# Optimization experiments

Measured on AMD Instinct MI355X. Metric: run time of the kernel, lower is better.

## Reference

```python
import jax, jax.numpy as jnp
import numpy as np

B, T, D, H, E, K, F = 8, 1024, 512, 8, 8, 2, 2048
HD = D // H
EPS = 1e-5


def _layernorm(x, g, b):
    m = jnp.mean(x, axis=-1, keepdims=True)
    v = jnp.mean((x - m) ** 2, axis=-1, keepdims=True)
    return (x - m) * jax.lax.rsqrt(v + EPS) * g + b


def setup_inputs() -> dict:
    key = jax.random.key(0)
    ks = jax.random.split(key, 12)
    s = lambda d: 1.0 / np.sqrt(d)
    return {
        "x": jax.random.normal(ks[0], (B, T, D), jnp.float32),
        "ln1_g": jnp.ones((D,), jnp.float32),
        "ln1_b": jnp.zeros((D,), jnp.float32),
        "ln2_g": jnp.ones((D,), jnp.float32),
        "ln2_b": jnp.zeros((D,), jnp.float32),
        "Wqkv": jax.random.normal(ks[1], (D, 3 * D), jnp.float32) * s(D),
        "bqkv": jnp.zeros((3 * D,), jnp.float32),
        "Wo": jax.random.normal(ks[2], (D, D), jnp.float32) * s(D),
        "bo": jnp.zeros((D,), jnp.float32),
        "Wg": jax.random.normal(ks[3], (D, E), jnp.float32) * s(D),
        "We1": jax.random.normal(ks[4], (E, D, F), jnp.float32) * s(D),
        "be1": jnp.zeros((E, F), jnp.float32),
        "We2": jax.random.normal(ks[5], (E, F, D), jnp.float32) * s(F),
        "be2": jnp.zeros((E, D), jnp.float32),
    }


def _attn(x, Wqkv, bqkv, Wo, bo):
    qkv = x @ Wqkv + bqkv                      # [B,T,3D]
    q, k, v = jnp.split(qkv, 3, axis=-1)
    q = q.reshape(B, T, H, HD)
    k = k.reshape(B, T, H, HD)
    v = v.reshape(B, T, H, HD)
    scores = jnp.einsum("bqhd,bkhd->bhqk", q, k) / np.sqrt(HD)
    causal = jnp.tril(jnp.ones((T, T), bool))
    scores = jnp.where(causal, scores, jnp.finfo(scores.dtype).min)
    p = jax.nn.softmax(scores, axis=-1)
    o = jnp.einsum("bhqk,bkhd->bqhd", p, v).reshape(B, T, D)
    return o @ Wo + bo


def _moe(h, Wg, We1, be1, We2, be2):
    hf = h.reshape(-1, D)                      # [N,D]
    N = hf.shape[0]
    probs = jax.nn.softmax(hf @ Wg, axis=-1)   # [N,E]
    topw, topi = jax.lax.top_k(probs, K)       # [N,K]
    topw = topw / jnp.sum(topw, axis=-1, keepdims=True)
    gates = jnp.zeros((N, E), hf.dtype).at[jnp.arange(N)[:, None], topi].add(topw)
    out = jnp.zeros_like(hf)
    for e in range(E):                         # fixed small expert loop
        hid = jax.nn.gelu(hf @ We1[e] + be1[e])
        out = out + gates[:, e:e + 1] * (hid @ We2[e] + be2[e])
    return out.reshape(h.shape)


def reference(x, ln1_g, ln1_b, ln2_g, ln2_b, Wqkv, bqkv, Wo, bo, Wg, We1, be1, We2, be2):
    # Pipeline chunking over batch is a scheduling detail; math is the plain block.
    h = x + _attn(_layernorm(x, ln1_g, ln1_b), Wqkv, bqkv, Wo, bo)
    return h + _moe(_layernorm(h, ln2_g, ln2_b), Wg, We1, be1, We2, be2)
```

## Files before the change

### kernel.cpp

```cpp
#include <hip/hip_runtime.h>


typedef unsigned short u16;
typedef unsigned int   u32;
typedef unsigned long long u64;
typedef __attribute__((ext_vector_type(8))) short short8;
typedef __attribute__((ext_vector_type(4))) float f32x4;

#define DEV static __device__ __forceinline__

DEV u16 f2bf(float f){
  union { float f; u32 u; } x; x.f = f;
  return (u16)((x.u + 0x7FFFu + ((x.u >> 16) & 1u)) >> 16);
}
DEV float bf2f(u16 b){
  union { u32 u; float f; } x; x.u = ((u32)b) << 16; return x.f;
}
DEV f32x4 mfma16(short8 a, short8 b, f32x4 c){
  return __builtin_amdgcn_mfma_f32_16x16x32_bf16(a, b, c, 0, 0, 0);
}
DEV void g2l16(const void* g, void* l){
  __builtin_amdgcn_global_load_lds((const __attribute__((address_space(1))) u32*)g,
                                   (__attribute__((address_space(3))) u32*)l, 16, 0, 0);
}
DEV void wait_vm0(){ asm volatile("s_waitcnt vmcnt(0)" ::: "memory"); }

__global__ __launch_bounds__(256) void transpose_cvt2(const float* __restrict__ src,
    u16* __restrict__ dh, u16* __restrict__ dl, int R, int C)
{
  __shared__ float tile[32][33];
  const size_t zb = (size_t)blockIdx.z * R * C;
  src += zb; dh += zb; dl += zb;
  const int tx = threadIdx.x, ty = threadIdx.y;
  const int c0 = blockIdx.x * 32, r0 = blockIdx.y * 32;
  #pragma unroll
  for (int i = 0; i < 4; ++i)
    tile[ty + i*8][tx] = src[(size_t)(r0 + ty + i*8) * C + c0 + tx];
  __syncthreads();
  #pragma unroll
  for (int i = 0; i < 4; ++i){
    float v = tile[tx][ty + i*8];
    size_t o = (size_t)(c0 + ty + i*8) * R + r0 + tx;
    u16 hb = f2bf(v);
    dh[o] = hb;
    dl[o] = f2bf(v - bf2f(hb));
  }
}

__global__ __launch_bounds__(256) void transpose_cvt1(const float* __restrict__ src,
    u16* __restrict__ d, int R, int C)
{
  __shared__ float tile[32][33];
  const size_t zb = (size_t)blockIdx.z * R * C;
  src += zb; d += zb;
  const int tx = threadIdx.x, ty = threadIdx.y;
  const int c0 = blockIdx.x * 32, r0 = blockIdx.y * 32;
  #pragma unroll
  for (int i = 0; i < 4; ++i)
    tile[ty + i*8][tx] = src[(size_t)(r0 + ty + i*8) * C + c0 + tx];
  __syncthreads();
  #pragma unroll
  for (int i = 0; i < 4; ++i)
    d[(size_t)(c0 + ty + i*8) * R + r0 + tx] = f2bf(tile[tx][ty + i*8]);
}

__global__ __launch_bounds__(256) void ln1_kernel(const float* __restrict__ x,
    const float* __restrict__ g, const float* __restrict__ b,
    u16* __restrict__ yh, u16* __restrict__ yl)
{
  const int wid = threadIdx.x >> 6, lane = threadIdx.x & 63;
  const int row = blockIdx.x * 4 + wid;
  const float* xr = x + (size_t)row * 512 + lane * 8;
  f32x4 t0 = ((const f32x4*)xr)[0], t1 = ((const f32x4*)xr)[1];
  float v[8];
  #pragma unroll
  for (int j = 0; j < 8; ++j) v[j] = (j < 4) ? t0[j] : t1[j-4];
  float s = 0.f, q = 0.f;
  #pragma unroll
  for (int j = 0; j < 8; ++j){ s += v[j]; q += v[j]*v[j]; }
  #pragma unroll
  for (int o = 32; o; o >>= 1){ s += __shfl_xor(s, o); q += __shfl_xor(q, o); }
  const float mean = s * (1.f/512.f);
  const float var  = q * (1.f/512.f) - mean*mean;
  const float rstd = rsqrtf(var + 1e-5f);
  f32x4 g0 = ((const f32x4*)(g + lane*8))[0], g1 = ((const f32x4*)(g + lane*8))[1];
  f32x4 b0 = ((const f32x4*)(b + lane*8))[0], b1 = ((const f32x4*)(b + lane*8))[1];
  short8 vh, vl;
  #pragma unroll
  for (int j = 0; j < 8; ++j){
    float gg = (j < 4) ? g0[j] : g1[j-4];
    float bb = (j < 4) ? b0[j] : b1[j-4];
    float y = (v[j]-mean)*rstd*gg + bb;
    u16 hb = f2bf(y);
    vh[j] = (short)hb;
    vl[j] = (short)f2bf(y - bf2f(hb));
  }
  ((short8*)(yh + (size_t)row*512 + lane*8))[0] = vh;
  ((short8*)(yl + (size_t)row*512 + lane*8))[0] = vl;
}

template<int MODE>
__global__ __launch_bounds__(256) void gemm_split2(
    const u16* __restrict__ Ah, const u16* __restrict__ Al,
    const u16* __restrict__ Bh, const u16* __restrict__ Bl,
    const float* __restrict__ bias, int K,
    u16* __restrict__ q_h, u16* __restrict__ q_l, u16* __restrict__ q_m,
    u16* __restrict__ k_h, u16* __restrict__ k_l, u16* __restrict__ k_m,
    u16* __restrict__ v_h, u16* __restrict__ v_l,
    const float* __restrict__ xres, float* __restrict__ hout)
{
  __shared__ u16 Ash[2][128*32], Asl[2][128*32], Bsh[2][128*32], Bsl[2][128*32];
  const int tid = threadIdx.x;
  const int wid = tid >> 6, lane = tid & 63;
  const int wr = wid >> 1, wc = wid & 1;
  const int lr = lane & 15, lg = lane >> 4;
  const int m0 = blockIdx.x * 128, n0 = blockIdx.y * 128;

  size_t aoff[2], boff[2];
  u32 ldso[2];
  #pragma unroll
  for (int r = 0; r < 2; ++r){
    int i = r*256 + tid;
    int row = i >> 2, cc = i & 3;
    int scc = cc ^ (row & 3);
    aoff[r] = ((size_t)(m0+row)*K + scc*8) * 2;
    boff[r] = ((size_t)(n0+row)*K + scc*8) * 2;
    ldso[r] = (u32)(r*256 + wid*64) * 8;
  }

  f32x4 acc[4][4];
  #pragma unroll
  for (int a = 0; a < 4; ++a)
    #pragma unroll
    for (int b = 0; b < 4; ++b) acc[a][b] = 0;

  const char* pAh = (const char*)Ah; const char* pAl = (const char*)Al;
  const char* pBh = (const char*)Bh; const char* pBl = (const char*)Bl;

  auto stage = [&](int sb, int ks){
    const size_t kb = (size_t)ks * 64;
    #pragma unroll
    for (int r = 0; r < 2; ++r){
      g2l16(pAh + aoff[r] + kb, &Ash[sb][0] + ldso[r]);
      g2l16(pAl + aoff[r] + kb, &Asl[sb][0] + ldso[r]);
      g2l16(pBh + boff[r] + kb, &Bsh[sb][0] + ldso[r]);
      g2l16(pBl + boff[r] + kb, &Bsl[sb][0] + ldso[r]);
    }
  };

  const int nks = K >> 5;
  stage(0, 0);
  wait_vm0();
  __syncthreads();
  int buf = 0;
  for (int ks = 0; ks < nks; ++ks){
    if (ks + 1 < nks) stage(buf ^ 1, ks + 1);
    short8 ah[4], al[4], bh[4], bl[4];
    #pragma unroll
    for (int mt = 0; mt < 4; ++mt){
      int row = wr*64 + mt*16 + lr;
      int kcs = lg ^ (row & 3);
      int o = row*32 + kcs*8;
      ah[mt] = *(const short8*)(&Ash[buf][0] + o);
      al[mt] = *(const short8*)(&Asl[buf][0] + o);
    }
    #pragma unroll
    for (int nt = 0; nt < 4; ++nt){
      int row = wc*64 + nt*16 + lr;
      int kcs = lg ^ (row & 3);
      int o = row*32 + kcs*8;
      bh[nt] = *(const short8*)(&Bsh[buf][0] + o);
      bl[nt] = *(const short8*)(&Bsl[buf][0] + o);
    }
    __builtin_amdgcn_s_setprio(1);
    #pragma unroll
    for (int mt = 0; mt < 4; ++mt)
      #pragma unroll
      for (int nt = 0; nt < 4; ++nt){
        f32x4 c = acc[mt][nt];
        c = mfma16(ah[mt], bh[nt], c);
        c = mfma16(ah[mt], bl[nt], c);
        c = mfma16(al[mt], bh[nt], c);
        acc[mt][nt] = c;
      }
    __builtin_amdgcn_s_setprio(0);
    wait_vm0();
    __syncthreads();
    buf ^= 1;
  }

  #pragma unroll
  for (int mt = 0; mt < 4; ++mt){
    #pragma unroll
    for (int nt = 0; nt < 4; ++nt){
      const int col = n0 + wc*64 + nt*16 + lr;
      const float bv = bias[col];
      #pragma unroll
      for (int r2 = 0; r2 < 4; ++r2){
        const int row = m0 + wr*64 + mt*16 + 4*lg + r2;
        const float val = acc[mt][nt][r2] + bv;
        if constexpr (MODE == 0){
          const int which = col >> 9, rem = col & 511;
          const int hh = rem >> 6, hd = rem & 63;
          const int b_ = row >> 10, t_ = row & 1023;
          const size_t idx = ((size_t)(b_*8 + hh)*1024 + t_)*64 + hd;
          const u16 hb = f2bf(val);
          if (which == 2){
            v_h[idx] = hb;
            v_l[idx] = f2bf(val - bf2f(hb));
          } else {
            const float r1 = val - bf2f(hb);
            const u16 lb = f2bf(r1);
            const u16 mb = f2bf(r1 - bf2f(lb));
            if (which == 0){ q_h[idx]=hb; q_l[idx]=lb; q_m[idx]=mb; }
            else           { k_h[idx]=hb; k_l[idx]=lb; k_m[idx]=mb; }
          }
        } else {
          const size_t o = (size_t)row*512 + col;
          hout[o] = val + xres[o];
        }
      }
    }
  }
}

__global__ __launch_bounds__(256) void attn_kernel(
    const u16* __restrict__ q_h, const u16* __restrict__ q_l, const u16* __restrict__ q_m,
    const u16* __restrict__ k_h, const u16* __restrict__ k_l, const u16* __restrict__ k_m,
    const u16* __restrict__ v_h, const u16* __restrict__ v_l,
    u16* __restrict__ aoh, u16* __restrict__ aol)
{
  __shared__ u16 Ksh[64*64], Ksl[64*64], Ksm[64*64];
  __shared__ u16 Vth[64*72], Vtl[64*72];
  __shared__ u16 Ph[4*16*72], Pl[4*16*72];
  const int tid = threadIdx.x, wid = tid >> 6, lane = tid & 63;
  const int lr = lane & 15, lg = lane >> 4;
  const int bfl = blockIdx.x;
  const int xcd = bfl & 7, jj_ = bfl >> 3;
  const int bh = xcd * 8 + (jj_ & 7);
  const int qt = 15 - (jj_ >> 3);
  const int q0 = qt * 64;
  const size_t base = (size_t)bh * 1024 * 64;

  short8 qfh[2], qfl[2], qfm[2];
  {
    const int qrow = q0 + wid*16 + lr;
    #pragma unroll
    for (int c = 0; c < 2; ++c){
      const size_t o = base + (size_t)qrow*64 + c*32 + lg*8;
      qfh[c] = *(const short8*)(q_h + o);
      qfl[c] = *(const short8*)(q_l + o);
      qfm[c] = *(const short8*)(q_m + o);
    }
  }
  f32x4 oacc[4];
  float m_r[4], l_r[4];
  #pragma unroll
  for (int nt = 0; nt < 4; ++nt) oacc[nt] = 0;
  #pragma unroll
  for (int r = 0; r < 4; ++r){ m_r[r] = -1e30f; l_r[r] = 0.f; }

  short8 kreg[3][2];
  short8 vreg[2][2];
  const int pp = tid & 31, d0 = (tid >> 5) * 8;

  auto load_tile = [&](int kt){
    #pragma unroll
    for (int r = 0; r < 2; ++r){
      const int i = r*256 + tid;
      const int row = i >> 3, cc = i & 7;
      const int scc = cc ^ (row & 7);
      const size_t go = base + (size_t)(kt*64 + row)*64 + scc*8;
      kreg[0][r] = *(const short8*)(k_h + go);
      kreg[1][r] = *(const short8*)(k_l + go);
      kreg[2][r] = *(const short8*)(k_m + go);
    }
    const size_t g0 = base + (size_t)(kt*64 + 2*pp)*64 + d0;
    vreg[0][0] = *(const short8*)(v_h + g0);
    vreg[0][1] = *(const short8*)(v_h + g0 + 64);
    vreg[1][0] = *(const short8*)(v_l + g0);
    vreg[1][1] = *(const short8*)(v_l + g0 + 64);
  };

  load_tile(0);
  for (int kt = 0; kt <= qt; ++kt){
    if (kt) __syncthreads();
    #pragma unroll
    for (int r = 0; r < 2; ++r){
      const int o = (r*256 + tid) * 8;
      *(short8*)(Ksh + o) = kreg[0][r];
      *(short8*)(Ksl + o) = kreg[1][r];
      *(short8*)(Ksm + o) = kreg[2][r];
    }
    #pragma unroll
    for (int j = 0; j < 8; ++j){
      u32 ph_ = (u32)(u16)vreg[0][0][j] | ((u32)(u16)vreg[0][1][j] << 16);
      u32 pl_ = (u32)(u16)vreg[1][0][j] | ((u32)(u16)vreg[1][1][j] << 16);
      *(u32*)(Vth + (d0+j)*72 + 2*pp) = ph_;
      *(u32*)(Vtl + (d0+j)*72 + 2*pp) = pl_;
    }
    __syncthreads();
    if (kt < qt) load_tile(kt + 1);
    __builtin_amdgcn_sched_barrier(0);

    f32x4 s[4];
    #pragma unroll
    for (int nt = 0; nt < 4; ++nt) s[nt] = 0;
    __builtin_amdgcn_s_setprio(1);
    #pragma unroll
    for (int c = 0; c < 2; ++c){
      #pragma unroll
      for (int nt = 0; nt < 4; ++nt){
        const int row = nt*16 + lr;
        const int kcs = (c*4 + lg) ^ (row & 7);
        const int o = row*64 + kcs*8;
        short8 kh_ = *(const short8*)(Ksh + o);
        short8 kl_ = *(const short8*)(Ksl + o);
        short8 km_ = *(const short8*)(Ksm + o);
        f32x4 cacc = s[nt];
        cacc = mfma16(qfh[c], kh_, cacc);
        cacc = mfma16(qfh[c], kl_, cacc);
        cacc = mfma16(qfl[c], kh_, cacc);
        cacc = mfma16(qfh[c], km_, cacc);
        cacc = mfma16(qfm[c], kh_, cacc);
        cacc = mfma16(qfl[c], kl_, cacc);
        s[nt] = cacc;
      }
    }
    __builtin_amdgcn_s_setprio(0);
    float sc[4][4];
    const bool last = (kt == qt);
    #pragma unroll
    for (int nt = 0; nt < 4; ++nt)
      #pragma unroll
      for (int r = 0; r < 4; ++r){
        float v = s[nt][r] * 0.125f;
        if (last){
          int qa = q0 + wid*16 + 4*lg + r;
          int ka = kt*64 + nt*16 + lr;
          if (ka > qa) v = -1e30f;
        }
        sc[nt][r] = v;
      }
    float pr[4][4];
    #pragma unroll
    for (int r = 0; r < 4; ++r){
      float mx = fmaxf(fmaxf(sc[0][r], sc[1][r]), fmaxf(sc[2][r], sc[3][r]));
      #pragma unroll
      for (int o2 = 8; o2; o2 >>= 1) mx = fmaxf(mx, __shfl_xor(mx, o2));
      const float nm = fmaxf(m_r[r], mx);
      const float al = __expf(m_r[r] - nm);
      float sum = 0.f;
      #pragma unroll
      for (int nt = 0; nt < 4; ++nt){
        float e_ = __expf(sc[nt][r] - nm);
        pr[nt][r] = e_;
        sum += e_;
      }
      #pragma unroll
      for (int o2 = 8; o2; o2 >>= 1) sum += __shfl_xor(sum, o2);
      l_r[r] = l_r[r]*al + sum;
      m_r[r] = nm;
      #pragma unroll
      for (int nt = 0; nt < 4; ++nt) oacc[nt][r] *= al;
    }
    #pragma unroll
    for (int nt = 0; nt < 4; ++nt)
      #pragma unroll
      for (int r = 0; r < 4; ++r){
        const float pv = pr[nt][r];
        const u16 hb = f2bf(pv);
        const u16 lb = f2bf(pv - bf2f(hb));
        const int o = wid*1152 + (4*lg + r)*72 + nt*16 + lr;
        Ph[o] = hb; Pl[o] = lb;
      }
    #pragma unroll
    for (int c = 0; c < 2; ++c){
      const int po = wid*1152 + lr*72 + c*32 + lg*8;
      short8 pah = *(const short8*)(Ph + po);
      short8 pal = *(const short8*)(Pl + po);
      __builtin_amdgcn_s_setprio(1);
      #pragma unroll
      for (int nt = 0; nt < 4; ++nt){
        const int vo = (nt*16 + lr)*72 + c*32 + lg*8;
        short8 vhf = *(const short8*)(Vth + vo);
        short8 vlf = *(const short8*)(Vtl + vo);
        f32x4 cacc = oacc[nt];
        cacc = mfma16(pah, vhf, cacc);
        cacc = mfma16(pah, vlf, cacc);
        cacc = mfma16(pal, vhf, cacc);
        oacc[nt] = cacc;
      }
      __builtin_amdgcn_s_setprio(0);
    }
  }

  const int b_ = bh >> 3, h_ = bh & 7;
  #pragma unroll
  for (int nt = 0; nt < 4; ++nt)
    #pragma unroll
    for (int r = 0; r < 4; ++r){
      const int qa = q0 + wid*16 + 4*lg + r;
      const float val = oacc[nt][r] / l_r[r];
      const size_t o = ((size_t)(b_*1024 + qa))*512 + h_*64 + nt*16 + lr;
      const u16 hb = f2bf(val);
      aoh[o] = hb;
      aol[o] = f2bf(val - bf2f(hb));
    }
}

__global__ __launch_bounds__(256) void ln2_gate_kernel(const float* __restrict__ h,
    const float* __restrict__ g, const float* __restrict__ b,
    const float* __restrict__ Wg, u16* __restrict__ y2,
    int* __restrict__ ge, float* __restrict__ gw)
{
  const int wid = threadIdx.x >> 6, lane = threadIdx.x & 63;
  const int row = blockIdx.x * 4 + wid;
  const float* xr = h + (size_t)row * 512 + lane * 8;
  f32x4 t0 = ((const f32x4*)xr)[0], t1 = ((const f32x4*)xr)[1];
  float v[8];
  #pragma unroll
  for (int j = 0; j < 8; ++j) v[j] = (j < 4) ? t0[j] : t1[j-4];
  float s = 0.f, q = 0.f;
  #pragma unroll
  for (int j = 0; j < 8; ++j){ s += v[j]; q += v[j]*v[j]; }
  #pragma unroll
  for (int o = 32; o; o >>= 1){ s += __shfl_xor(s, o); q += __shfl_xor(q, o); }
  const float mean = s * (1.f/512.f);
  const float var  = q * (1.f/512.f) - mean*mean;
  const float rstd = rsqrtf(var + 1e-5f);
  f32x4 g0 = ((const f32x4*)(g + lane*8))[0], g1 = ((const f32x4*)(g + lane*8))[1];
  f32x4 b0 = ((const f32x4*)(b + lane*8))[0], b1 = ((const f32x4*)(b + lane*8))[1];
  float yv[8];
  short8 yb;
  #pragma unroll
  for (int j = 0; j < 8; ++j){
    float gg = (j < 4) ? g0[j] : g1[j-4];
    float bb = (j < 4) ? b0[j] : b1[j-4];
    yv[j] = (v[j]-mean)*rstd*gg + bb;
    yb[j] = (short)f2bf(yv[j]);
  }
  ((short8*)(y2 + (size_t)row*512 + lane*8))[0] = yb;

  float lgt[8];
  #pragma unroll
  for (int e = 0; e < 8; ++e) lgt[e] = 0.f;
  #pragma unroll
  for (int j = 0; j < 8; ++j){
    const float* wr_ = Wg + (size_t)(lane*8 + j) * 8;
    #pragma unroll
    for (int e = 0; e < 8; ++e) lgt[e] += yv[j] * wr_[e];
  }
  #pragma unroll
  for (int o = 32; o; o >>= 1){
    #pragma unroll
    for (int e = 0; e < 8; ++e) lgt[e] += __shfl_xor(lgt[e], o);
  }
  if (lane == 0){
    int e0 = 0; float l0 = lgt[0];
    #pragma unroll
    for (int e = 1; e < 8; ++e) if (lgt[e] > l0){ l0 = lgt[e]; e0 = e; }
    int e1 = -1; float l1 = -3e38f;
    #pragma unroll
    for (int e = 0; e < 8; ++e) if (e != e0 && lgt[e] > l1){ l1 = lgt[e]; e1 = e; }
    const float t = expf(l1 - l0);
    const float w0 = 1.f / (1.f + t);
    const float w1 = t * w0;
    ge[row*2]   = e0; ge[row*2+1] = e1;
    gw[row*2]   = w0; gw[row*2+1] = w1;
  }
}

__global__ __launch_bounds__(256) void count_kernel(const int* __restrict__ ge,
                                                    int* __restrict__ cnt)
{
  const int i = blockIdx.x * 256 + threadIdx.x;
  const int lane = threadIdx.x & 63;
  const int e = ge[i];
  #pragma unroll
  for (int ex = 0; ex < 8; ++ex){
    u64 m = __ballot(e == ex);
    if (m && lane == (int)(__ffsll((long long)m) - 1))
      atomicAdd(&cnt[ex], __popcll(m));
  }
}

__global__ void offsets_kernel(int* cnt){
  if (threadIdx.x == 0){
    int o = 0, tp = 0;
    for (int e = 0; e < 8; ++e){
      cnt[8+e] = o; cnt[17+e] = o;
      cnt[25+e] = tp;
      o  += cnt[e];
      tp += (cnt[e] + 127) >> 7;
    }
    cnt[16] = o;
    cnt[33] = tp;
  }
}

__global__ __launch_bounds__(256) void scatter_kernel(const int* __restrict__ ge,
    const float* __restrict__ gw, int* __restrict__ cnt,
    int* __restrict__ rdst, float* __restrict__ rw)
{
  const int i = blockIdx.x * 256 + threadIdx.x;
  const int lane = threadIdx.x & 63;
  const int e = ge[i];
  const float w = gw[i];
  const u64 below = ((u64)1 << lane) - 1;
  int pos = -1;
  #pragma unroll
  for (int ex = 0; ex < 8; ++ex){
    u64 m = __ballot(e == ex);
    if (m){
      const int leader = (int)(__ffsll((long long)m) - 1);
      int base = 0;
      if (lane == leader) base = atomicAdd(&cnt[17 + ex], __popcll(m));
      base = __shfl(base, leader);
      if (e == ex) pos = base + __popcll(m & below);
    }
  }
  rdst[pos] = i;
  rw[pos]   = w;
}

template<int MODE>
__global__ __launch_bounds__(256) void gemm_moe(
    const u16* __restrict__ A, const u16* __restrict__ Bt,
    const float* __restrict__ bias, int N, int K,
    const int* __restrict__ cntblk,
    const int* __restrict__ rdst, const float* __restrict__ rw,
    u16* __restrict__ hid, float* __restrict__ contrib)
{
  __shared__ u16 As[2][128*64], Bs[2][128*64];
  const int bx = blockIdx.x;
  if (bx >= cntblk[33]) return;
  int e = 7;
  #pragma unroll
  for (int k = 7; k >= 1; --k) if (bx < cntblk[25 + k]) e = k - 1;
  const int ce = cntblk[e];
  const int eo = cntblk[8 + e];
  const int m0 = (bx - cntblk[25 + e]) * 128;

  const int tid = threadIdx.x;
  const int wid = tid >> 6, lane = tid & 63;
  const int wr = wid >> 1, wc = wid & 1;
  const int lr = lane & 15, lg = lane >> 4;
  const int n0 = blockIdx.y * 128;

  size_t aoff[4], boff[4];
  u32 ldso[4];
  #pragma unroll
  for (int r = 0; r < 4; ++r){
    int i = r*256 + tid;
    int row = i >> 3, cc = i & 7;
    int scc = cc ^ (row & 7);
    int p = eo + m0 + row;
    const int pmax = eo + ce - 1;
    if (p > pmax) p = pmax;
    const int arow = (MODE == 2) ? (rdst[p] >> 1) : p;
    aoff[r] = ((size_t)arow * K + scc*8) * 2;
    boff[r] = (((size_t)e * N + n0 + row) * K + scc*8) * 2;
    ldso[r] = (u32)(r*256 + wid*64) * 8;
  }

  f32x4 acc[4][4];
  #pragma unroll
  for (int a = 0; a < 4; ++a)
    #pragma unroll
    for (int b = 0; b < 4; ++b) acc[a][b] = 0;

  const char* pA = (const char*)A;
  const char* pB = (const char*)Bt;

  auto stage = [&](int sb, int ks){
    const size_t kb = (size_t)ks * 128;
    #pragma unroll
    for (int r = 0; r < 4; ++r){
      g2l16(pA + aoff[r] + kb, &As[sb][0] + ldso[r]);
      g2l16(pB + boff[r] + kb, &Bs[sb][0] + ldso[r]);
    }
  };

  const int nks = K >> 6;
  stage(0, 0);
  wait_vm0();
  __syncthreads();
  int buf = 0;
  for (int ks = 0; ks < nks; ++ks){
    if (ks + 1 < nks) stage(buf ^ 1, ks + 1);
    #pragma unroll
    for (int kk = 0; kk < 2; ++kk){
      short8 av[4], bv[4];
      #pragma unroll
      for (int mt = 0; mt < 4; ++mt){
        int row = wr*64 + mt*16 + lr;
        int kcs = (kk*4 + lg) ^ (row & 7);
        av[mt] = *(const short8*)(&As[buf][0] + row*64 + kcs*8);
      }
      #pragma unroll
      for (int nt = 0; nt < 4; ++nt){
        int row = wc*64 + nt*16 + lr;
        int kcs = (kk*4 + lg) ^ (row & 7);
        bv[nt] = *(const short8*)(&Bs[buf][0] + row*64 + kcs*8);
      }
      __builtin_amdgcn_s_setprio(1);
      #pragma unroll
      for (int mt = 0; mt < 4; ++mt)
        #pragma unroll
        for (int nt = 0; nt < 4; ++nt)
          acc[mt][nt] = mfma16(av[mt], bv[nt], acc[mt][nt]);
      __builtin_amdgcn_s_setprio(0);
    }
    wait_vm0();
    __syncthreads();
    buf ^= 1;
  }

  const float* bp = bias + (size_t)e * N;
  #pragma unroll
  for (int mt = 0; mt < 4; ++mt){
    #pragma unroll
    for (int nt = 0; nt < 4; ++nt){
      const int col = n0 + wc*64 + nt*16 + lr;
      const float bv2 = bp[col];
      #pragma unroll
      for (int r2 = 0; r2 < 4; ++r2){
        const int lrow = wr*64 + mt*16 + 4*lg + r2;
        if (m0 + lrow < ce){
          const int p = eo + m0 + lrow;
          const float val = acc[mt][nt][r2] + bv2;
          if constexpr (MODE == 2){
            const float gx = val;
            const float gl = 0.5f * gx * (1.f + tanhf(0.7978845608028654f * (gx + 0.044715f*gx*gx*gx)));
            hid[(size_t)p * N + col] = f2bf(gl);
          } else {
            contrib[(size_t)rdst[p] * N + col] = val * rw[p];
          }
        }
      }
    }
  }
}

__global__ __launch_bounds__(256) void final_kernel(const float* __restrict__ h,
    const float* __restrict__ contrib, float* __restrict__ out)
{
  const int i = blockIdx.x * 256 + threadIdx.x;
  const int row = i >> 7, rem = i & 127;
  const f32x4* c4 = (const f32x4*)contrib;
  f32x4 hv = ((const f32x4*)h)[i];
  f32x4 a = c4[(size_t)(row*2) * 128 + rem];
  f32x4 b = c4[(size_t)(row*2) * 128 + 128 + rem];
  ((f32x4*)out)[i] = hv + a + b;
}

extern "C" void kernel_launch(void* const* d_in, const int* in_sizes, int n_in,
                              void* d_out, int out_size, void* d_ws, size_t ws_size,
                              hipStream_t stream)
{
  (void)in_sizes; (void)n_in; (void)out_size; (void)ws_size;
  const float* x    = (const float*)d_in[0];
  const float* ln1g = (const float*)d_in[1];
  const float* ln1b = (const float*)d_in[2];
  const float* ln2g = (const float*)d_in[3];
  const float* ln2b = (const float*)d_in[4];
  const float* Wqkv = (const float*)d_in[5];
  const float* bqkv = (const float*)d_in[6];
  const float* Wo   = (const float*)d_in[7];
  const float* bo   = (const float*)d_in[8];
  const float* Wg   = (const float*)d_in[9];
  const float* We1  = (const float*)d_in[10];
  const float* be1  = (const float*)d_in[11];
  const float* We2  = (const float*)d_in[12];
  const float* be2  = (const float*)d_in[13];
  float* out = (float*)d_out;

  char* ws = (char*)d_ws;
  size_t off_ = 0;
  auto alloc = [&](size_t bytes)->char*{
    char* p = ws + off_;
    off_ = (off_ + bytes + 255) & ~(size_t)255;
    return p;
  };
  u16* wqkvTh = (u16*)alloc((size_t)1536*512*2);
  u16* wqkvTl = (u16*)alloc((size_t)1536*512*2);
  u16* woTh   = (u16*)alloc((size_t)512*512*2);
  u16* woTl   = (u16*)alloc((size_t)512*512*2);
  u16* we1T   = (u16*)alloc((size_t)8*2048*512*2);
  u16* we2T   = (u16*)alloc((size_t)8*512*2048*2);
  u16* y1h    = (u16*)alloc((size_t)8192*512*2);
  u16* y1l    = (u16*)alloc((size_t)8192*512*2);
  u16* qh_    = (u16*)alloc((size_t)8192*64*8*2);
  u16* ql_    = (u16*)alloc((size_t)8192*64*8*2);
  u16* qm_    = (u16*)alloc((size_t)8192*64*8*2);
  u16* kh_    = (u16*)alloc((size_t)8192*64*8*2);
  u16* kl_    = (u16*)alloc((size_t)8192*64*8*2);
  u16* km_    = (u16*)alloc((size_t)8192*64*8*2);
  u16* vh_    = (u16*)alloc((size_t)8192*64*8*2);
  u16* vl_    = (u16*)alloc((size_t)8192*64*8*2);
  u16* aoh    = (u16*)alloc((size_t)8192*512*2);
  u16* aol    = (u16*)alloc((size_t)8192*512*2);
  float* hbuf = (float*)alloc((size_t)8192*512*4);
  u16* y2     = (u16*)alloc((size_t)8192*512*2);
  int* ge     = (int*)alloc((size_t)8192*2*4);
  float* gw   = (float*)alloc((size_t)8192*2*4);
  int* cnt    = (int*)alloc(256);
  int* rdst   = (int*)alloc((size_t)16384*4);
  float* rw   = (float*)alloc((size_t)16384*4);
  u16* hid    = (u16*)alloc((size_t)16384*2048*2);
  float* contrib = (float*)alloc((size_t)16384*512*4);

  (void)hipMemsetAsync(cnt, 0, 256, stream);

  const dim3 tb(32, 8);
  transpose_cvt2<<<dim3(48, 16, 1), tb, 0, stream>>>(Wqkv, wqkvTh, wqkvTl, 512, 1536);
  transpose_cvt2<<<dim3(16, 16, 1), tb, 0, stream>>>(Wo,   woTh,   woTl,   512, 512);
  transpose_cvt1<<<dim3(64, 16, 8), tb, 0, stream>>>(We1, we1T, 512, 2048);
  transpose_cvt1<<<dim3(16, 64, 8), tb, 0, stream>>>(We2, we2T, 2048, 512);

  ln1_kernel<<<2048, 256, 0, stream>>>(x, ln1g, ln1b, y1h, y1l);

  gemm_split2<0><<<dim3(64, 12), 256, 0, stream>>>(
      y1h, y1l, wqkvTh, wqkvTl, bqkv, 512,
      qh_, ql_, qm_, kh_, kl_, km_, vh_, vl_, nullptr, nullptr);

  attn_kernel<<<dim3(1024), 256, 0, stream>>>(
      qh_, ql_, qm_, kh_, kl_, km_, vh_, vl_, aoh, aol);

  gemm_split2<1><<<dim3(64, 4), 256, 0, stream>>>(
      aoh, aol, woTh, woTl, bo, 512,
      nullptr, nullptr, nullptr, nullptr, nullptr, nullptr, nullptr, nullptr,
      x, hbuf);

  ln2_gate_kernel<<<2048, 256, 0, stream>>>(hbuf, ln2g, ln2b, Wg, y2, ge, gw);
  count_kernel<<<64, 256, 0, stream>>>(ge, cnt);
  offsets_kernel<<<1, 64, 0, stream>>>(cnt);
  scatter_kernel<<<64, 256, 0, stream>>>(ge, gw, cnt, rdst, rw);

  gemm_moe<2><<<dim3(135, 16), 256, 0, stream>>>(
      y2, we1T, be1, 2048, 512, cnt, rdst, rw, hid, nullptr);
  gemm_moe<3><<<dim3(135, 4), 256, 0, stream>>>(
      hid, we2T, be2, 512, 2048, cnt, rdst, rw, nullptr, contrib);

  final_kernel<<<4096, 256, 0, stream>>>(hbuf, contrib, out);
}
```

Measured before the change: 511.9 us.

## Remap MoE GEMM blocks into XCD-aware M-bands and use exp-based GELU

The 2D grid of the expert GEMMs becomes a flat 1D grid. Each block index is decoded so that consecutive blocks on the same XCD (fid & 7) cover a band of M tiles across all N tiles. The goal is better L2 reuse of A rows and expert weights within each XCD's cache. The tanh GELU is also replaced by the algebraically equivalent x*sigmoid(2z) form using __expf, which makes the epilogue cheaper. The grid is enlarged (3072 and 640 blocks), so more blocks exit early, and the fast exp adds slight numeric differences.

```diff
diff --git a/kernel.cpp b/kernel.cpp
--- a/kernel.cpp
+++ b/kernel.cpp
@@ -524,7 +524,7 @@
   rw[pos]   = w;
 }
 
-template<int MODE>
+template<int MODE, int TN, int BAND_M, int BPX>
 __global__ __launch_bounds__(256) void gemm_moe(
     const u16* __restrict__ A, const u16* __restrict__ Bt,
     const float* __restrict__ bias, int N, int K,
@@ -533,20 +533,28 @@
     u16* __restrict__ hid, float* __restrict__ contrib)
 {
   __shared__ u16 As[2][128*64], Bs[2][128*64];
-  const int bx = blockIdx.x;
-  if (bx >= cntblk[33]) return;
+  const int fid = blockIdx.x;
+  const int xcd = fid & 7;
+  const int j   = fid >> 3;
+  const int bpb = BAND_M * TN;
+  const int bi  = j / bpb;
+  const int r_  = j % bpb;
+  const int nt_ = r_ / BAND_M;
+  const int mi  = r_ % BAND_M;
+  const int mt  = (xcd * BPX + bi) * BAND_M + mi;
+  if (mt >= cntblk[33]) return;
   int e = 7;
   #pragma unroll
-  for (int k = 7; k >= 1; --k) if (bx < cntblk[25 + k]) e = k - 1;
+  for (int k = 7; k >= 1; --k) if (mt < cntblk[25 + k]) e = k - 1;
   const int ce = cntblk[e];
   const int eo = cntblk[8 + e];
-  const int m0 = (bx - cntblk[25 + e]) * 128;
+  const int m0 = (mt - cntblk[25 + e]) * 128;
+  const int n0 = nt_ * 128;
 
   const int tid = threadIdx.x;
   const int wid = tid >> 6, lane = tid & 63;
   const int wr = wid >> 1, wc = wid & 1;
   const int lr = lane & 15, lg = lane >> 4;
-  const int n0 = blockIdx.y * 128;
 
   size_t aoff[4], boff[4];
   u32 ldso[4];
@@ -593,23 +601,23 @@
     for (int kk = 0; kk < 2; ++kk){
       short8 av[4], bv[4];
       #pragma unroll
-      for (int mt = 0; mt < 4; ++mt){
-        int row = wr*64 + mt*16 + lr;
+      for (int mt2 = 0; mt2 < 4; ++mt2){
+        int row = wr*64 + mt2*16 + lr;
         int kcs = (kk*4 + lg) ^ (row & 7);
-        av[mt] = *(const short8*)(&As[buf][0] + row*64 + kcs*8);
-      }
-      #pragma unroll
-      for (int nt = 0; nt < 4; ++nt){
-        int row = wc*64 + nt*16 + lr;
+        av[mt2] = *(const short8*)(&As[buf][0] + row*64 + kcs*8);
+      }
+      #pragma unroll
+      for (int nt2 = 0; nt2 < 4; ++nt2){
+        int row = wc*64 + nt2*16 + lr;
         int kcs = (kk*4 + lg) ^ (row & 7);
-        bv[nt] = *(const short8*)(&Bs[buf][0] + row*64 + kcs*8);
+        bv[nt2] = *(const short8*)(&Bs[buf][0] + row*64 + kcs*8);
       }
       __builtin_amdgcn_s_setprio(1);
       #pragma unroll
-      for (int mt = 0; mt < 4; ++mt)
+      for (int mt2 = 0; mt2 < 4; ++mt2)
         #pragma unroll
-        for (int nt = 0; nt < 4; ++nt)
-          acc[mt][nt] = mfma16(av[mt], bv[nt], acc[mt][nt]);
+        for (int nt2 = 0; nt2 < 4; ++nt2)
+          acc[mt2][nt2] = mfma16(av[mt2], bv[nt2], acc[mt2][nt2]);
       __builtin_amdgcn_s_setprio(0);
     }
     wait_vm0();
@@ -619,20 +627,21 @@
 
   const float* bp = bias + (size_t)e * N;
   #pragma unroll
-  for (int mt = 0; mt < 4; ++mt){
-    #pragma unroll
-    for (int nt = 0; nt < 4; ++nt){
-      const int col = n0 + wc*64 + nt*16 + lr;
+  for (int mt2 = 0; mt2 < 4; ++mt2){
+    #pragma unroll
+    for (int nt2 = 0; nt2 < 4; ++nt2){
+      const int col = n0 + wc*64 + nt2*16 + lr;
       const float bv2 = bp[col];
       #pragma unroll
       for (int r2 = 0; r2 < 4; ++r2){
-        const int lrow = wr*64 + mt*16 + 4*lg + r2;
+        const int lrow = wr*64 + mt2*16 + 4*lg + r2;
         if (m0 + lrow < ce){
           const int p = eo + m0 + lrow;
-          const float val = acc[mt][nt][r2] + bv2;
+          const float val = acc[mt2][nt2][r2] + bv2;
           if constexpr (MODE == 2){
             const float gx = val;
-            const float gl = 0.5f * gx * (1.f + tanhf(0.7978845608028654f * (gx + 0.044715f*gx*gx*gx)));
+            const float z2 = 1.5957691216057308f * (gx + 0.044715f*gx*gx*gx);
+            const float gl = gx / (1.f + __expf(-z2));
             hid[(size_t)p * N + col] = f2bf(gl);
           } else {
             contrib[(size_t)rdst[p] * N + col] = val * rw[p];
@@ -738,9 +747,9 @@
   offsets_kernel<<<1, 64, 0, stream>>>(cnt);
   scatter_kernel<<<64, 256, 0, stream>>>(ge, gw, cnt, rdst, rw);
 
-  gemm_moe<2><<<dim3(135, 16), 256, 0, stream>>>(
+  gemm_moe<2, 16, 8, 3><<<dim3(3072), 256, 0, stream>>>(
       y2, we1T, be1, 2048, 512, cnt, rdst, rw, hid, nullptr);
-  gemm_moe<3><<<dim3(135, 4), 256, 0, stream>>>(
+  gemm_moe<3, 4, 4, 5><<<dim3(640), 256, 0, stream>>>(
       hid, we2T, be2, 512, 2048, cnt, rdst, rw, nullptr, contrib);
 
   final_kernel<<<4096, 256, 0, stream>>>(hbuf, contrib, out);
```

Result: faster. 491.8 us (-3.9%).
